# Performance work log

Hardware: AMD Instinct MI355X
Metric: run time of the kernel (lower is better)

The kernel has to match this reference:

```python
import jax, jax.numpy as jnp
import numpy as np

B, R, N, E, DIN, DOUT = 2, 2, 50000, 500000, 128, 128


def setup_inputs() -> dict:
    key = jax.random.key(0)
    k_x, k_src, k_dst, k_val, k_w = jax.random.split(key, 5)
    x = jax.random.normal(k_x, (B, N, DIN), dtype=jnp.float32)
    edge_src = jax.random.randint(k_src, (B, R, E), 0, N, dtype=jnp.int32)
    edge_dst = jax.random.randint(k_dst, (B, R, E), 0, N, dtype=jnp.int32)
    edge_val = jax.random.uniform(k_val, (B, R, E), dtype=jnp.float32)
    # Glorot-uniform init as in init_weight: range = sqrt(6/(fan_in+fan_out))
    init_range = float(np.sqrt(6.0 / (DIN + DOUT)))
    weights = jax.random.uniform(k_w, (R, DIN, DOUT), minval=-init_range,
                                 maxval=init_range, dtype=jnp.float32)
    bias = jnp.zeros((DOUT,), dtype=jnp.float32)
    return {"x": x, "edge_val": edge_val, "weights": weights, "bias": bias,
            "edge_src": edge_src, "edge_dst": edge_dst}


def reference(x, edge_val, weights, bias, edge_src, edge_dst):
    # Dense feature transform per relation: pre_sup = x @ W_r  -> [B, R, N, DOUT]
    pre = jnp.einsum('bnd,rde->brne', x, weights)
    bi = jnp.arange(B)[:, None, None]   # [B,1,1]
    ri = jnp.arange(R)[None, :, None]   # [1,R,1]
    # Sparse adjacency matmul A_r @ pre_sup:
    # out[dst] += A[dst, src] * pre_sup[src]  (edge list form)
    msgs = edge_val[..., None] * pre[bi, ri, edge_src]          # [B,R,E,DOUT]
    agg = jnp.zeros((B, R, N, DOUT), dtype=pre.dtype)
    agg = agg.at[bi, ri, edge_dst].add(msgs)                    # scatter-add
    # Sum across relations (tf.add_n), add bias, relu activation
    out = agg.sum(axis=1) + bias                                # [B,N,DOUT]
    return jax.nn.relu(out)
```

## Files before the change

kernel.cpp:

```cpp
#include <hip/hip_runtime.h>

#define BB 2
#define RR 2
#define NN 50000
#define EE 500000
#define DD 128
#define NSLOT 4
#define BSH 6
#define BSZ 64
#define NB 782
#define FT 8192
#define FBLK 62
#define SCAP 2048
#define DSTR 50048
#define CASTB 3125

#define C_XB   0u
#define C_REC  25600000u
#define C_CNT  33600000u
#define C_OFS  33612512u
#define C_CUR  33625056u
#define C_DOF  33637568u
#define C_WT   34438336u
#define C_TOTAL 34503872u

#define A_XB   0u
#define A_REC  12800000u
#define A_CNT  20800000u
#define A_OFS  20812544u
#define A_CUR  20825088u
#define A_DOF  20837632u
#define A_WT   21638400u

typedef __attribute__((ext_vector_type(8))) short bf16x8;
typedef __attribute__((ext_vector_type(4))) float f32x4;

__device__ __forceinline__ unsigned short f2bf(float f) {
    unsigned int u = __float_as_uint(f);
    u += 0x7fffu + ((u >> 16) & 1u);
    return (unsigned short)(u >> 16);
}

__device__ __forceinline__ bf16x8 pack8(float4 a, float4 b) {
    bf16x8 r;
    r[0] = (short)f2bf(a.x); r[1] = (short)f2bf(a.y);
    r[2] = (short)f2bf(a.z); r[3] = (short)f2bf(a.w);
    r[4] = (short)f2bf(b.x); r[5] = (short)f2bf(b.y);
    r[6] = (short)f2bf(b.z); r[7] = (short)f2bf(b.w);
    return r;
}

__global__ __launch_bounds__(256) void prep_kernel(
    const float* __restrict__ x, unsigned short* __restrict__ xb,
    const int* __restrict__ edst, int* __restrict__ counts,
    const float* __restrict__ w, unsigned short* __restrict__ wt2)
{
    __shared__ int h[NB];
    const int blk = blockIdx.x;
    const int tid = threadIdx.x;
    if (blk < 512) {
        for (int i = tid; i < NB; i += 256) h[i] = 0;
        __syncthreads();
        const int slot = blk >> 7;
        const int* ed = edst + (size_t)slot * EE;
        for (int e = (blk & 127) * 256 + tid; e < EE; e += 128 * 256)
            atomicAdd(&h[ed[e] >> BSH], 1);
        __syncthreads();
        int* c = counts + slot * NB;
        for (int i = tid; i < NB; i += 256) {
            int v = h[i];
            if (v) atomicAdd(&c[i], v);
        }
    } else if (blk < 512 + 2 * CASTB) {
        const size_t i8 = (size_t)(blk - 512) * 2048 + (size_t)tid * 8;
        float4 v0 = *(const float4*)&x[i8];
        float4 v1 = *(const float4*)&x[i8 + 4];
        *(bf16x8*)&xb[i8] = pack8(v0, v1);
    } else {
        int idx = (blk - 512 - 2 * CASTB) * 256 + tid;
        int r = idx >> 14;
        int k = (idx >> 7) & (DD - 1);
        int n = idx & (DD - 1);
        wt2[(size_t)n * 256 + r * DD + k] = f2bf(w[idx]);
    }
}

__global__ __launch_bounds__(256) void wprep_kernel(
    const float* __restrict__ w, unsigned short* __restrict__ wt2)
{
    int idx = blockIdx.x * 256 + threadIdx.x;
    if (idx >= RR * DD * DD) return;
    int r = idx >> 14;
    int k = (idx >> 7) & (DD - 1);
    int n = idx & (DD - 1);
    wt2[(size_t)n * 256 + r * DD + k] = f2bf(w[idx]);
}

__global__ __launch_bounds__(256) void cast_kernel(
    const float* __restrict__ x, unsigned short* __restrict__ xb)
{
    const size_t bo = (size_t)blockIdx.y * NN * DD;
    int i8 = (blockIdx.x * 256 + threadIdx.x) * 8;
    if (i8 >= NN * DD) return;
    float4 v0 = *(const float4*)&x[bo + i8];
    float4 v1 = *(const float4*)&x[bo + i8 + 4];
    *(bf16x8*)&xb[bo + i8] = pack8(v0, v1);
}

__global__ __launch_bounds__(256) void hist_kernel(
    const int* __restrict__ edst, int* __restrict__ counts)
{
    __shared__ int h[NB];
    for (int i = threadIdx.x; i < NB; i += 256) h[i] = 0;
    __syncthreads();
    const int slot = blockIdx.y;
    const int* ed = edst + (size_t)slot * EE;
    for (int e = blockIdx.x * 256 + threadIdx.x; e < EE; e += 128 * 256)
        atomicAdd(&h[ed[e] >> BSH], 1);
    __syncthreads();
    int* c = counts + slot * NB;
    for (int i = threadIdx.x; i < NB; i += 256) {
        int v = h[i];
        if (v) atomicAdd(&c[i], v);
    }
}

__global__ __launch_bounds__(1024) void scan_kernel(
    const int* __restrict__ counts, int* __restrict__ offsets,
    int* __restrict__ cursor)
{
    __shared__ int s[1024];
    const int slot = blockIdx.x;
    int v = (threadIdx.x < NB) ? counts[slot * NB + threadIdx.x] : 0;
    s[threadIdx.x] = v;
    for (int o = 1; o < 1024; o <<= 1) {
        __syncthreads();
        int t = (threadIdx.x >= o) ? s[threadIdx.x - o] : 0;
        __syncthreads();
        s[threadIdx.x] += t;
    }
    __syncthreads();
    if (threadIdx.x < NB) {
        int incl = s[threadIdx.x];
        offsets[slot * 784 + threadIdx.x + 1] = incl;
        cursor[slot * NB + threadIdx.x] = incl - v;
    }
    if (threadIdx.x == 0) offsets[slot * 784] = 0;
}

__global__ __launch_bounds__(1024) void fill_kernel(
    const int* __restrict__ esrc, const int* __restrict__ edst,
    const float* __restrict__ ev, int* __restrict__ cursor,
    unsigned int* __restrict__ recs)
{
    __shared__ int lh[NB];
    __shared__ int lbase[NB];
    const int slot = blockIdx.y;
    const size_t eb = (size_t)slot * EE;
    const int e0 = blockIdx.x * FT;

    for (int i = threadIdx.x; i < NB; i += 1024) lh[i] = 0;
    __syncthreads();
    for (int t = 0; t < FT; t += 1024) {
        int e = e0 + t + threadIdx.x;
        if (e < EE) atomicAdd(&lh[edst[eb + e] >> BSH], 1);
    }
    __syncthreads();
    for (int i = threadIdx.x; i < NB; i += 1024) {
        int c = lh[i];
        lbase[i] = c ? atomicAdd(&cursor[slot * NB + i], c) : 0;
        lh[i] = 0;
    }
    __syncthreads();
    for (int t = 0; t < FT; t += 1024) {
        int e = e0 + t + threadIdx.x;
        if (e < EE) {
            int d = edst[eb + e];
            int bk = d >> BSH;
            unsigned vq = (unsigned)__builtin_rintf(ev[eb + e] * 1023.0f);
            unsigned rec = (unsigned)esrc[eb + e] |
                           ((unsigned)(d & (BSZ - 1)) << 16) | (vq << 22);
            int p = lbase[bk] + atomicAdd(&lh[bk], 1);
            recs[eb + p] = rec;
        }
    }
}

#define DEQ (1.0f / 1023.0f)

__global__ __launch_bounds__(256) void sort_kernel(
    unsigned int* __restrict__ recs, const int* __restrict__ offsets,
    int* __restrict__ dofs)
{
    __shared__ unsigned int lrec[SCAP];
    __shared__ int cnt[BSZ];
    __shared__ int cur[BSZ];
    const int bk = blockIdx.x, slot = blockIdx.y;
    unsigned int* rp = recs + (size_t)slot * EE;
    const int s = offsets[slot * 784 + bk], e = offsets[slot * 784 + bk + 1];
    const int n = e - s;

    for (int i = threadIdx.x; i < n; i += 256) lrec[i] = rp[s + i];
    if (threadIdx.x < BSZ) cnt[threadIdx.x] = 0;
    __syncthreads();
    for (int i = threadIdx.x; i < n; i += 256)
        atomicAdd(&cnt[(lrec[i] >> 16) & (BSZ - 1)], 1);
    __syncthreads();
    if (threadIdx.x < 64) {
        int v = cnt[threadIdx.x];
        int incl = v;
        #pragma unroll
        for (int o = 1; o < 64; o <<= 1) {
            int t = __shfl_up(incl, o, 64);
            if (threadIdx.x >= o) incl += t;
        }
        int excl = incl - v;
        cur[threadIdx.x] = excl;
        dofs[(size_t)slot * DSTR + bk * BSZ + threadIdx.x] = s + excl;
    }
    __syncthreads();
    for (int i = threadIdx.x; i < n; i += 256) {
        unsigned r = lrec[i];
        int p = atomicAdd(&cur[(r >> 16) & (BSZ - 1)], 1);
        float v = (float)(r >> 22) * DEQ;
        rp[s + p] = (r & 0xffffu) | ((unsigned)f2bf(v) << 16);
    }
}

#define LO16(u) __uint_as_float((u) << 16)
#define HI16(u) __uint_as_float((u) & 0xffff0000u)

__device__ __forceinline__ void gacc2(const unsigned short* __restrict__ xb,
                                      const unsigned int* __restrict__ rp,
                                      unsigned i, unsigned e,
                                      unsigned half, unsigned lane4,
                                      float acc[4])
{
    for (; i + 8 <= e; i += 8) {
        unsigned q[4]; uint2 u[4];
        #pragma unroll
        for (int j = 0; j < 4; ++j) q[j] = rp[i + 2 * j + half];
        #pragma unroll
        for (int j = 0; j < 4; ++j)
            u[j] = *(const uint2*)(xb + (((q[j] & 0xffffu) << 7) + lane4));
        #pragma unroll
        for (int j = 0; j < 4; ++j) {
            float s = __uint_as_float(q[j] & 0xffff0000u);
            acc[0] = fmaf(s, LO16(u[j].x), acc[0]);
            acc[1] = fmaf(s, HI16(u[j].x), acc[1]);
            acc[2] = fmaf(s, LO16(u[j].y), acc[2]);
            acc[3] = fmaf(s, HI16(u[j].y), acc[3]);
        }
    }
    for (; i + 2 <= e; i += 2) {
        unsigned q = rp[i + half];
        uint2 u = *(const uint2*)(xb + (((q & 0xffffu) << 7) + lane4));
        float s = __uint_as_float(q & 0xffff0000u);
        acc[0] = fmaf(s, LO16(u.x), acc[0]);
        acc[1] = fmaf(s, HI16(u.x), acc[1]);
        acc[2] = fmaf(s, LO16(u.y), acc[2]);
        acc[3] = fmaf(s, HI16(u.y), acc[3]);
    }
    if (i < e && half == 0) {
        unsigned q = rp[i];
        uint2 u = *(const uint2*)(xb + (((q & 0xffffu) << 7) + lane4));
        float s = __uint_as_float(q & 0xffff0000u);
        acc[0] = fmaf(s, LO16(u.x), acc[0]);
        acc[1] = fmaf(s, HI16(u.x), acc[1]);
        acc[2] = fmaf(s, LO16(u.y), acc[2]);
        acc[3] = fmaf(s, HI16(u.y), acc[3]);
    }
}

__global__ __launch_bounds__(256) void gather_dual_kernel(
    const unsigned short* __restrict__ xb,
    const unsigned int* __restrict__ recs,
    const int* __restrict__ dofs,
    float* __restrict__ out)
{
    const int y = blockIdx.y;
    const unsigned short* xbb = xb + (size_t)y * NN * DD;
    const unsigned int* rp0 = recs + (size_t)(y * 2) * EE;
    const unsigned int* rp1 = rp0 + EE;
    const int* d0p = dofs + (size_t)(y * 2) * DSTR;
    const int* d1p = d0p + DSTR;
    unsigned short* agg = (unsigned short*)(out + (size_t)y * NN * DD);

    const int d = blockIdx.x * 4 + (threadIdx.x >> 6);
    const int lane = threadIdx.x & 63;
    const unsigned half = (unsigned)(lane >> 5);
    const unsigned lane4 = (unsigned)(lane & 31) * 4;

    float a[4] = {0.f, 0.f, 0.f, 0.f};
    float b[4] = {0.f, 0.f, 0.f, 0.f};
    gacc2(xbb, rp0, d0p[d], d0p[d + 1], half, lane4, a);
    gacc2(xbb, rp1, d1p[d], d1p[d + 1], half, lane4, b);

    #pragma unroll
    for (int k = 0; k < 4; ++k) {
        a[k] += __shfl_xor(a[k], 32);
        b[k] += __shfl_xor(b[k], 32);
    }

    float s0 = half ? b[0] : a[0];
    float s1 = half ? b[1] : a[1];
    float s2 = half ? b[2] : a[2];
    float s3 = half ? b[3] : a[3];
    uint2 pv;
    pv.x = (unsigned)f2bf(s0) | ((unsigned)f2bf(s1) << 16);
    pv.y = (unsigned)f2bf(s2) | ((unsigned)f2bf(s3) << 16);
    *(uint2*)(agg + (size_t)d * 256 + half * DD + lane4) = pv;
}

__global__ __launch_bounds__(256) void gemm_agg_kernel(
    const unsigned short* __restrict__ wt2,
    const float* __restrict__ bias,
    float* __restrict__ out)
{
    float* outb = out + (size_t)blockIdx.y * NN * DD;
    const unsigned short* agg = (const unsigned short*)outb;
    const int tid = threadIdx.x;
    const int w = tid >> 6, lane = tid & 63;
    const int wr = w >> 1, wc = w & 1;
    const int lq = lane >> 4, lr = lane & 15;
    const int row0 = blockIdx.x * 128;

    f32x4 acc[4][4] = {};

    #pragma unroll
    for (int ks = 0; ks < 8; ++ks) {
        const int k0 = ks * 32 + lq * 8;
        bf16x8 a[4], b[4];
        #pragma unroll
        for (int mi = 0; mi < 4; ++mi) {
            int row = row0 + wr * 64 + mi * 16 + lr;
            bf16x8 v = {};
            if (row < NN) v = *(const bf16x8*)(agg + (size_t)row * 256 + k0);
            a[mi] = v;
        }
        #pragma unroll
        for (int ni = 0; ni < 4; ++ni) {
            int n = wc * 64 + ni * 16 + lr;
            b[ni] = *(const bf16x8*)(wt2 + (size_t)n * 256 + k0);
        }
        #pragma unroll
        for (int mi = 0; mi < 4; ++mi)
            #pragma unroll
            for (int ni = 0; ni < 4; ++ni)
                acc[mi][ni] = __builtin_amdgcn_mfma_f32_16x16x32_bf16(
                    a[mi], b[ni], acc[mi][ni], 0, 0, 0);
    }

    __syncthreads();

    #pragma unroll
    for (int mi = 0; mi < 4; ++mi) {
        #pragma unroll
        for (int q = 0; q < 4; ++q) {
            int row = row0 + wr * 64 + mi * 16 + lq * 4 + q;
            if (row < NN) {
                #pragma unroll
                for (int ni = 0; ni < 4; ++ni) {
                    int col = wc * 64 + ni * 16 + lr;
                    outb[(size_t)row * DD + col] =
                        fmaxf(acc[mi][ni][q] + bias[col], 0.f);
                }
            }
        }
    }
}

extern "C" void kernel_launch(void* const* d_in, const int* in_sizes, int n_in,
                              void* d_out, int out_size, void* d_ws, size_t ws_size,
                              hipStream_t stream) {
    const float* x     = (const float*)d_in[0];
    const float* eval_ = (const float*)d_in[1];
    const float* w     = (const float*)d_in[2];
    const float* bias  = (const float*)d_in[3];
    const int*   esrc  = (const int*)d_in[4];
    const int*   edst  = (const int*)d_in[5];
    float* out = (float*)d_out;

    const bool useC = (ws_size >= (size_t)C_TOTAL);

    char* ws = (char*)d_ws;
    unsigned short* xb      = (unsigned short*)(ws + (useC ? C_XB : A_XB));
    unsigned int*   recs    = (unsigned int*)(ws + (useC ? C_REC : A_REC));
    int*            counts  = (int*)(ws + (useC ? C_CNT : A_CNT));
    int*            offsets = (int*)(ws + (useC ? C_OFS : A_OFS));
    int*            cursor  = (int*)(ws + (useC ? C_CUR : A_CUR));
    int*            dofs    = (int*)(ws + (useC ? C_DOF : A_DOF));
    unsigned short* wt2     = (unsigned short*)(ws + (useC ? C_WT : A_WT));

    const dim3 blk(256);
    const dim3 gath_grid(NN / 4);
    const dim3 gemm_grid((NN + 127) / 128);

    hipMemsetAsync(counts, 0, NSLOT * NB * sizeof(int), stream);

    if (useC) {
        prep_kernel<<<512 + 2 * CASTB + 128, blk, 0, stream>>>(
            x, xb, edst, counts, w, wt2);
        scan_kernel<<<dim3(NSLOT), dim3(1024), 0, stream>>>(
            counts, offsets, cursor);
        fill_kernel<<<dim3(FBLK, NSLOT), dim3(1024), 0, stream>>>(
            esrc, edst, eval_, cursor, recs);
        sort_kernel<<<dim3(NB, NSLOT), blk, 0, stream>>>(recs, offsets, dofs);
        gather_dual_kernel<<<dim3(gath_grid.x, BB), blk, 0, stream>>>(
            xb, recs, dofs, out);
        gemm_agg_kernel<<<dim3(gemm_grid.x, BB), blk, 0, stream>>>(
            wt2, bias, out);
    } else {
        wprep_kernel<<<(RR * DD * DD + 255) / 256, blk, 0, stream>>>(w, wt2);
        hist_kernel<<<dim3(128, NSLOT), blk, 0, stream>>>(edst, counts);
        scan_kernel<<<dim3(NSLOT), dim3(1024), 0, stream>>>(
            counts, offsets, cursor);
        fill_kernel<<<dim3(FBLK, NSLOT), dim3(1024), 0, stream>>>(
            esrc, edst, eval_, cursor, recs);
        sort_kernel<<<dim3(NB, NSLOT), blk, 0, stream>>>(recs, offsets, dofs);
        const dim3 cast_grid((NN * DD / 8 + 255) / 256);
        for (int b = 0; b < BB; ++b) {
            cast_kernel<<<cast_grid, blk, 0, stream>>>(
                x + (size_t)b * NN * DD, xb);
            gather_dual_kernel<<<gath_grid, blk, 0, stream>>>(
                xb, recs + (size_t)(b * 2) * EE, dofs + (size_t)(b * 2) * DSTR,
                out + (size_t)b * NN * DD);
            gemm_agg_kernel<<<gemm_grid, blk, 0, stream>>>(
                wt2, bias, out + (size_t)b * NN * DD);
        }
    }
}
```

Measured before the change: 181.4 us.

## Fuse gather aggregation and weight GEMM into one kernel via LDS tile

Replaces the separate gather and GEMM kernels in the main path with one kernel. Each block aggregates 16 destination rows for both relations into a bf16 tile in shared memory, then runs MFMA against the stacked weights and writes bias-added ReLU output directly. This removes the global write and re-read of the intermediate bf16 aggregate buffer and one kernel launch. The cost is smaller GEMM tiles, which reload the weight matrix from L2 for every 16 rows, plus a block-wide barrier after the irregular gather. The secondary path now uses the per-batch gather and GEMM kernels with pointer offsets passed by the host.

```diff
diff --git a/kernel.cpp b/kernel.cpp
--- a/kernel.cpp
+++ b/kernel.cpp
@@ -14,6 +14,8 @@
 #define SCAP 2048
 #define DSTR 50048
 #define CASTB 3125
+#define GROWS 16
+#define LSTR 264
 
 #define C_XB   0u
 #define C_REC  25600000u
@@ -272,19 +274,88 @@
     }
 }
 
-__global__ __launch_bounds__(256) void gather_dual_kernel(
+__global__ __launch_bounds__(256) void gather_gemm_kernel(
     const unsigned short* __restrict__ xb,
     const unsigned int* __restrict__ recs,
     const int* __restrict__ dofs,
+    const unsigned short* __restrict__ wt2,
+    const float* __restrict__ bias,
     float* __restrict__ out)
 {
+    __shared__ unsigned short agg[GROWS * LSTR];
+
     const int y = blockIdx.y;
     const unsigned short* xbb = xb + (size_t)y * NN * DD;
     const unsigned int* rp0 = recs + (size_t)(y * 2) * EE;
     const unsigned int* rp1 = rp0 + EE;
     const int* d0p = dofs + (size_t)(y * 2) * DSTR;
     const int* d1p = d0p + DSTR;
-    unsigned short* agg = (unsigned short*)(out + (size_t)y * NN * DD);
+
+    const int tid = threadIdx.x;
+    const int w = tid >> 6, lane = tid & 63;
+    const unsigned half = (unsigned)(lane >> 5);
+    const unsigned lane4 = (unsigned)(lane & 31) * 4;
+    const int dbase = blockIdx.x * GROWS;
+
+    #pragma unroll 1
+    for (int dd = 0; dd < 4; ++dd) {
+        const int d = dbase + w * 4 + dd;
+        float a[4] = {0.f, 0.f, 0.f, 0.f};
+        float b[4] = {0.f, 0.f, 0.f, 0.f};
+        gacc2(xbb, rp0, d0p[d], d0p[d + 1], half, lane4, a);
+        gacc2(xbb, rp1, d1p[d], d1p[d + 1], half, lane4, b);
+        #pragma unroll
+        for (int k = 0; k < 4; ++k) {
+            a[k] += __shfl_xor(a[k], 32);
+            b[k] += __shfl_xor(b[k], 32);
+        }
+        float s0 = half ? b[0] : a[0];
+        float s1 = half ? b[1] : a[1];
+        float s2 = half ? b[2] : a[2];
+        float s3 = half ? b[3] : a[3];
+        uint2 pv;
+        pv.x = (unsigned)f2bf(s0) | ((unsigned)f2bf(s1) << 16);
+        pv.y = (unsigned)f2bf(s2) | ((unsigned)f2bf(s3) << 16);
+        *(uint2*)(agg + (w * 4 + dd) * LSTR + half * DD + lane4) = pv;
+    }
+    __syncthreads();
+
+    const int lq = lane >> 4, lr = lane & 15;
+    f32x4 acc0 = {}, acc1 = {};
+    #pragma unroll
+    for (int ks = 0; ks < 8; ++ks) {
+        const int k0 = ks * 32 + lq * 8;
+        bf16x8 af = *(const bf16x8*)(agg + lr * LSTR + k0);
+        const int n0 = w * 32 + lr;
+        bf16x8 bf0 = *(const bf16x8*)(wt2 + (size_t)n0 * 256 + k0);
+        bf16x8 bf1 = *(const bf16x8*)(wt2 + (size_t)(n0 + 16) * 256 + k0);
+        acc0 = __builtin_amdgcn_mfma_f32_16x16x32_bf16(af, bf0, acc0, 0, 0, 0);
+        acc1 = __builtin_amdgcn_mfma_f32_16x16x32_bf16(af, bf1, acc1, 0, 0, 0);
+    }
+    float* outb = out + (size_t)y * NN * DD;
+    const int col0 = w * 32 + lr;
+    const float bz0 = bias[col0];
+    const float bz1 = bias[col0 + 16];
+    #pragma unroll
+    for (int q = 0; q < 4; ++q) {
+        const size_t row = (size_t)(dbase + lq * 4 + q);
+        outb[row * DD + col0]      = fmaxf(acc0[q] + bz0, 0.f);
+        outb[row * DD + col0 + 16] = fmaxf(acc1[q] + bz1, 0.f);
+    }
+}
+
+__global__ __launch_bounds__(256) void gather_dual_kernel(
+    const unsigned short* __restrict__ xb,
+    const unsigned int* __restrict__ recs,
+    const int* __restrict__ dofs,
+    float* __restrict__ out)
+{
+    const unsigned short* xbb = xb;
+    const unsigned int* rp0 = recs;
+    const unsigned int* rp1 = rp0 + EE;
+    const int* d0p = dofs;
+    const int* d1p = d0p + DSTR;
+    unsigned short* agg = (unsigned short*)out;
 
     const int d = blockIdx.x * 4 + (threadIdx.x >> 6);
     const int lane = threadIdx.x & 63;
@@ -295,13 +366,11 @@
     float b[4] = {0.f, 0.f, 0.f, 0.f};
     gacc2(xbb, rp0, d0p[d], d0p[d + 1], half, lane4, a);
     gacc2(xbb, rp1, d1p[d], d1p[d + 1], half, lane4, b);
-
     #pragma unroll
     for (int k = 0; k < 4; ++k) {
         a[k] += __shfl_xor(a[k], 32);
         b[k] += __shfl_xor(b[k], 32);
     }
-
     float s0 = half ? b[0] : a[0];
     float s1 = half ? b[1] : a[1];
     float s2 = half ? b[2] : a[2];
@@ -315,9 +384,8 @@
 __global__ __launch_bounds__(256) void gemm_agg_kernel(
     const unsigned short* __restrict__ wt2,
     const float* __restrict__ bias,
-    float* __restrict__ out)
-{
-    float* outb = out + (size_t)blockIdx.y * NN * DD;
+    float* __restrict__ outb)
+{
     const unsigned short* agg = (const unsigned short*)outb;
     const int tid = threadIdx.x;
     const int w = tid >> 6, lane = tid & 63;
@@ -393,8 +461,6 @@
     unsigned short* wt2     = (unsigned short*)(ws + (useC ? C_WT : A_WT));
 
     const dim3 blk(256);
-    const dim3 gath_grid(NN / 4);
-    const dim3 gemm_grid((NN + 127) / 128);
 
     hipMemsetAsync(counts, 0, NSLOT * NB * sizeof(int), stream);
 
@@ -406,10 +472,8 @@
         fill_kernel<<<dim3(FBLK, NSLOT), dim3(1024), 0, stream>>>(
             esrc, edst, eval_, cursor, recs);
         sort_kernel<<<dim3(NB, NSLOT), blk, 0, stream>>>(recs, offsets, dofs);
-        gather_dual_kernel<<<dim3(gath_grid.x, BB), blk, 0, stream>>>(
-            xb, recs, dofs, out);
-        gemm_agg_kernel<<<dim3(gemm_grid.x, BB), blk, 0, stream>>>(
-            wt2, bias, out);
+        gather_gemm_kernel<<<dim3(NN / GROWS, BB), blk, 0, stream>>>(
+            xb, recs, dofs, wt2, bias, out);
     } else {
         wprep_kernel<<<(RR * DD * DD + 255) / 256, blk, 0, stream>>>(w, wt2);
         hist_kernel<<<dim3(128, NSLOT), blk, 0, stream>>>(edst, counts);
@@ -419,6 +483,8 @@
             esrc, edst, eval_, cursor, recs);
         sort_kernel<<<dim3(NB, NSLOT), blk, 0, stream>>>(recs, offsets, dofs);
         const dim3 cast_grid((NN * DD / 8 + 255) / 256);
+        const dim3 gath_grid(NN / 4);
+        const dim3 gemm_grid((NN + 127) / 128);
         for (int b = 0; b < BB; ++b) {
             cast_kernel<<<cast_grid, blk, 0, stream>>>(
                 x + (size_t)b * NN * DD, xb);
```

Result: slower. 189.2 us (+4.3%).
